# Kernel tuning notes

Hardware: AMD Instinct MI355X
Metric: run time of the kernel (lower is better)

Reference implementation:

```python
import jax, jax.numpy as jnp
import numpy as np

N_NODES = 100000
N_EDGES = 1600000
F = 64          # node_features (in == out for EvolveGCNO)
HID = 64        # hidden_size


def setup_inputs() -> dict:
    key = jax.random.key(0)
    ks = jax.random.split(key, 12)
    s = 1.0 / np.sqrt(F)
    inp = {
        "x": jax.random.normal(ks[0], (N_NODES, F), dtype=jnp.float32),
        "edge_index": jax.random.randint(ks[1], (2, N_EDGES), 0, N_NODES, dtype=jnp.int64),
        "edge_weight": jax.random.uniform(ks[2], (N_EDGES,), dtype=jnp.float32),
        # evolving GCN weight (initial_weight of EvolveGCNO)
        "W0": jax.random.uniform(ks[3], (F, F), jnp.float32, -s, s),
        # GRU (input_size=F, hidden_size=F): gates ordered r, z, n
        "gru_Wi": jax.random.uniform(ks[4], (3 * F, F), jnp.float32, -s, s),
        "gru_Wh": jax.random.uniform(ks[5], (3 * F, F), jnp.float32, -s, s),
        "gru_bi": jax.random.uniform(ks[6], (3 * F,), jnp.float32, -s, s),
        "gru_bh": jax.random.uniform(ks[7], (3 * F,), jnp.float32, -s, s),
        # projection F -> HID and head HID -> 1
        "proj_W": jax.random.uniform(ks[8], (HID, F), jnp.float32, -s, s),
        "proj_b": jax.random.uniform(ks[9], (HID,), jnp.float32, -s, s),
        "lin_W": jax.random.uniform(ks[10], (1, HID), jnp.float32, -1.0 / np.sqrt(HID), 1.0 / np.sqrt(HID)),
        "lin_b": jax.random.uniform(ks[11], (1,), jnp.float32, -1.0 / np.sqrt(HID), 1.0 / np.sqrt(HID)),
    }
    return inp


def reference(x, edge_index, edge_weight, W0, gru_Wi, gru_Wh, gru_bi, gru_bh,
              proj_W, proj_b, lin_W, lin_b):
    N = x.shape[0]
    # --- EvolveGCNO weight evolution: one GRU step, rows of W0 are both input and hidden ---
    gi = W0 @ gru_Wi.T + gru_bi  # [F, 3F]
    gh = W0 @ gru_Wh.T + gru_bh  # [F, 3F]
    i_r, i_z, i_n = jnp.split(gi, 3, axis=1)
    h_r, h_z, h_n = jnp.split(gh, 3, axis=1)
    r = jax.nn.sigmoid(i_r + h_r)
    z = jax.nn.sigmoid(i_z + h_z)
    n = jnp.tanh(i_n + r * h_n)
    W = (1.0 - z) * n + z * W0  # evolved GCN weight [F, F]

    # --- GCNConv with fixed evolved W: X' = D^-1/2 (A + I) D^-1/2 (X W) ---
    xw = x @ W  # [N, F]
    src, dst = edge_index[0], edge_index[1]
    loop = jnp.arange(N)
    src2 = jnp.concatenate([src, loop])
    dst2 = jnp.concatenate([dst, loop])
    w2 = jnp.concatenate([edge_weight, jnp.ones((N,), xw.dtype)])  # self-loop weight 1
    deg = jax.ops.segment_sum(w2, dst2, num_segments=N)
    dinv = jnp.where(deg > 0, jax.lax.rsqrt(deg), 0.0)
    norm = dinv[src2] * w2 * dinv[dst2]  # [E + N]
    h = jax.ops.segment_sum(xw[src2] * norm[:, None], dst2, num_segments=N)  # [N, F]

    # --- MLP head (dropout is identity in eval) ---
    h = jax.nn.relu(h @ proj_W.T + proj_b)
    return h @ lin_W.T + lin_b  # [N, 1]
```

## Files before the change

### kernel.cpp

```cpp
#include <hip/hip_runtime.h>
#include <stdint.h>

#define FDIM 64
#define BINSH 6
#define NBINS 1563
#define BCAP 1536
#define OVCAP 8192
#define PSTAGE 8192
#define PBLK 196
#define LSTRIDE 72

__device__ __forceinline__ float bf2f(unsigned int u) {
    union { float f; uint32_t i; } v; v.i = (u & 0xFFFFu) << 16; return v.f;
}
__device__ __forceinline__ unsigned short f2bf(float f) {
    union { float f; uint32_t i; } v; v.f = f;
    uint32_t u = v.i;
    u += 0x7FFFu + ((u >> 16) & 1u);
    return (unsigned short)(u >> 16);
}

__global__ __launch_bounds__(256) void k_sentinel(float* out, int N, float val) {
    int n = blockIdx.x * 256 + threadIdx.x;
    if (n < N) out[n] = (n == 0) ? val : 0.f;
}

__global__ __launch_bounds__(1024) void k_prep(
    const int* __restrict__ src, const int* __restrict__ dst,
    const float* __restrict__ ew, int* __restrict__ gcnt,
    int2* __restrict__ part, int* __restrict__ ovf_cnt,
    int* __restrict__ ovs, int* __restrict__ ovd, float* __restrict__ ovw, int E,
    const float* __restrict__ W0, const float* __restrict__ Wi,
    const float* __restrict__ Wh, const float* __restrict__ bi,
    const float* __restrict__ bh, const float* __restrict__ projW,
    float* __restrict__ M) {
    __shared__ char sm[12504];
    int t = threadIdx.x;
    if (blockIdx.x < PBLK) {
        int* hist = (int*)sm;
        int* lcur = hist + NBINS;
        for (int b = t; b < NBINS; b += 1024) hist[b] = 0;
        __syncthreads();
        int e0 = blockIdx.x * PSTAGE;
        int cnt = E - e0; if (cnt > PSTAGE) cnt = PSTAGE;
        for (int i = t; i < cnt; i += 1024) atomicAdd(&hist[dst[e0 + i] >> BINSH], 1);
        __syncthreads();
        for (int b = t; b < NBINS; b += 1024) {
            int h = hist[b];
            lcur[b] = h ? atomicAdd(&gcnt[b], h) : 0;
        }
        __syncthreads();
        for (int i = t; i < cnt; i += 1024) {
            int e = e0 + i;
            int d = dst[e];
            int b = d >> BINSH;
            int p = atomicAdd(&lcur[b], 1);
            if (p < BCAP) {
                part[(size_t)b * BCAP + p] = make_int2(src[e] | ((d & 63) << 20),
                                                       __float_as_int(ew[e]));
            } else {
                int op = atomicAdd(ovf_cnt, 1);
                if (op < OVCAP) {
                    ovs[op] = src[e];
                    ovd[op] = d;
                    ovw[op] = ew[e];
                }
            }
        }
    } else {
        int i = blockIdx.x - PBLK;
        float* w0s  = (float*)sm;
        float* wrow = w0s + 64;
        if (t < 64) w0s[t] = W0[i * 64 + t];
        __syncthreads();
        if (t < 64) {
            int j = t;
            float a0 = 0.f, a1 = 0.f, a2 = 0.f, b0 = 0.f, b1 = 0.f, b2 = 0.f;
#pragma unroll 8
            for (int k = 0; k < 64; k++) {
                float w0k = w0s[k];
                a0 += w0k * Wi[(j)       * 64 + k];
                a1 += w0k * Wi[(64 + j)  * 64 + k];
                a2 += w0k * Wi[(128 + j) * 64 + k];
                b0 += w0k * Wh[(j)       * 64 + k];
                b1 += w0k * Wh[(64 + j)  * 64 + k];
                b2 += w0k * Wh[(128 + j) * 64 + k];
            }
            float ir = a0 + bi[j],        hr = b0 + bh[j];
            float iz = a1 + bi[64 + j],   hz = b1 + bh[64 + j];
            float in_ = a2 + bi[128 + j], hn = b2 + bh[128 + j];
            float r = 1.f / (1.f + expf(-(ir + hr)));
            float z = 1.f / (1.f + expf(-(iz + hz)));
            float n = tanhf(in_ + r * hn);
            wrow[j] = (1.f - z) * n + z * w0s[j];
        }
        __syncthreads();
        if (t < 64) {
            float s = 0.f;
#pragma unroll 8
            for (int q = 0; q < 64; q++) s += wrow[q] * projW[t * 64 + q];
            M[i * 64 + t] = s;
        }
    }
}

__global__ __launch_bounds__(256) void k_xmdeg(
    const float* __restrict__ x, const float* __restrict__ M,
    unsigned short* __restrict__ xm, int N,
    const int* __restrict__ gcnt, const int2* __restrict__ part,
    const int* __restrict__ ovf_cnt, const int* __restrict__ ovd,
    const float* __restrict__ ovw, float* __restrict__ dinv,
    int* __restrict__ loffg) {
    __shared__ char sm[34816];
    int t = threadIdx.x;
    if (blockIdx.x < NBINS) {
        float* xs = (float*)sm;
        float* ms = xs + 64 * 68;
        int nb = blockIdx.x * 64;
#pragma unroll
        for (int i = 0; i < 4; i++) {
            int lin = i * 1024 + t * 4;
            int row = lin >> 6, col = lin & 63;
            int node = nb + row;
            float4 v = make_float4(0.f, 0.f, 0.f, 0.f);
            if (node < N) v = *(const float4*)(x + (size_t)node * 64 + col);
            *(float4*)&xs[row * 68 + col] = v;
            *(float4*)&ms[row * 68 + col] = *(const float4*)(M + lin);
        }
        __syncthreads();
        int tj = t & 15, tn = t >> 4;
        float acc[4][4] = {};
        for (int k = 0; k < 64; k += 4) {
            float4 xv[4], mv[4];
#pragma unroll
            for (int nn = 0; nn < 4; nn++) xv[nn] = *(const float4*)&xs[(tn * 4 + nn) * 68 + k];
#pragma unroll
            for (int kk = 0; kk < 4; kk++) mv[kk] = *(const float4*)&ms[(k + kk) * 68 + tj * 4];
#pragma unroll
            for (int nn = 0; nn < 4; nn++) {
                const float* xp = (const float*)&xv[nn];
#pragma unroll
                for (int kk = 0; kk < 4; kk++) {
                    float xk = xp[kk];
                    const float* mp = (const float*)&mv[kk];
                    acc[nn][0] += xk * mp[0];
                    acc[nn][1] += xk * mp[1];
                    acc[nn][2] += xk * mp[2];
                    acc[nn][3] += xk * mp[3];
                }
            }
        }
#pragma unroll
        for (int nn = 0; nn < 4; nn++) {
            int node = nb + tn * 4 + nn;
            if (node < N) {
                ushort4 o;
                o.x = f2bf(acc[nn][0]); o.y = f2bf(acc[nn][1]);
                o.z = f2bf(acc[nn][2]); o.w = f2bf(acc[nn][3]);
                *(ushort4*)&xm[(size_t)node * 64 + tj * 4] = o;
            }
        }
    } else {
        int b = blockIdx.x - NBINS;
        float* dl   = (float*)sm;
        int*   cntl = (int*)(dl + 64);
        int*   lofl = cntl + 64;
        if (t < 64) { dl[t] = 1.0f; cntl[t] = 0; }
        __syncthreads();
        int c = gcnt[b]; if (c > BCAP) c = BCAP;
        const int2* pe = part + (size_t)b * BCAP;
        for (int i = t; i < c; i += 256) {
            int2 e = pe[i];
            int nl = (e.x >> 20) & 63;
            atomicAdd(&dl[nl], __int_as_float(e.y));
            atomicAdd(&cntl[nl], 1);
        }
        int m = *ovf_cnt; if (m > OVCAP) m = OVCAP;
        for (int i = t; i < m; i += 256) {
            int d = ovd[i];
            if ((d >> BINSH) == b) atomicAdd(&dl[d & 63], ovw[i]);
        }
        __syncthreads();
        if (t == 0) {
            int o = 0;
#pragma unroll 16
            for (int k = 0; k < 64; k++) { lofl[k] = o; o += cntl[k]; }
            lofl[64] = o;
        }
        __syncthreads();
        if (t < 64) {
            int n = b * 64 + t;
            if (n < N) dinv[n] = rsqrtf(dl[t]);
        }
        if (t < 65) loffg[b * LSTRIDE + t] = lofl[t];
    }
}

__global__ __launch_bounds__(256) void k_gf(
    const unsigned short* __restrict__ xm, const float* __restrict__ dinv,
    const int* __restrict__ gcnt, const int2* __restrict__ part,
    const int* __restrict__ loffg,
    const float* __restrict__ projB, const float* __restrict__ linW,
    const float* __restrict__ linB, const int* __restrict__ ovf_cnt,
    const int* __restrict__ ovs, const int* __restrict__ ovd,
    const float* __restrict__ ovw, float* __restrict__ out, int N) {
    __shared__ int  loff[65];
    __shared__ int  lcur[64];
    __shared__ int2 ledge[BCAP];
    __shared__ float pbs[64], lws[64];
    int t = threadIdx.x, b = blockIdx.x;
    if (t < 65) loff[t] = loffg[b * LSTRIDE + t];
    if (t < 64) { pbs[t] = projB[t]; lws[t] = linW[t]; }
    __syncthreads();
    if (t < 64) lcur[t] = loff[t];
    __syncthreads();
    int c = gcnt[b]; if (c > BCAP) c = BCAP;
    const int2* pe = part + (size_t)b * BCAP;
    for (int i = t; i < c; i += 256) {
        int2 e = pe[i];
        int s = e.x & 0xFFFFF;
        float nw = dinv[s] * __int_as_float(e.y);
        int p = atomicAdd(&lcur[(e.x >> 20) & 63], 1);
        ledge[p] = make_int2(e.x, __float_as_int(nw));
    }
    __syncthreads();
    int m = *ovf_cnt; if (m > OVCAP) m = OVCAP;
    float lb = linB[0];
    int wv = t >> 6, lane = t & 63, eg = lane >> 4, fq = lane & 15, f = fq * 4;
    for (int nl = wv; nl < 64; nl += 4) {
        int n = b * 64 + nl;
        if (n >= N) continue;
        float dn = dinv[n];
        int beg = loff[nl], end = loff[nl + 1];
        float ax = 0.f, ay = 0.f, az = 0.f, aw = 0.f;
        float bx = 0.f, by = 0.f, bz = 0.f, bw = 0.f;
        int i = beg + eg;
        for (; i + 4 < end; i += 8) {
            int2 e0 = ledge[i];
            int2 e1 = ledge[i + 4];
            int s0 = e0.x & 0xFFFFF, s1 = e1.x & 0xFFFFF;
            uint2 u0 = *(const uint2*)&xm[(size_t)s0 * 64 + f];
            uint2 u1 = *(const uint2*)&xm[(size_t)s1 * 64 + f];
            float nm0 = __int_as_float(e0.y);
            float nm1 = __int_as_float(e1.y);
            ax += nm0 * bf2f(u0.x);       ay += nm0 * bf2f(u0.x >> 16);
            az += nm0 * bf2f(u0.y);       aw += nm0 * bf2f(u0.y >> 16);
            bx += nm1 * bf2f(u1.x);       by += nm1 * bf2f(u1.x >> 16);
            bz += nm1 * bf2f(u1.y);       bw += nm1 * bf2f(u1.y >> 16);
        }
        for (; i < end; i += 4) {
            int2 e = ledge[i];
            int s = e.x & 0xFFFFF;
            float nm = __int_as_float(e.y);
            uint2 u = *(const uint2*)&xm[(size_t)s * 64 + f];
            ax += nm * bf2f(u.x); ay += nm * bf2f(u.x >> 16);
            az += nm * bf2f(u.y); aw += nm * bf2f(u.y >> 16);
        }
        ax += bx; ay += by; az += bz; aw += bw;
        ax *= dn; ay *= dn; az *= dn; aw *= dn;
        ax += __shfl_xor(ax, 16); ay += __shfl_xor(ay, 16);
        az += __shfl_xor(az, 16); aw += __shfl_xor(aw, 16);
        ax += __shfl_xor(ax, 32); ay += __shfl_xor(ay, 32);
        az += __shfl_xor(az, 32); aw += __shfl_xor(aw, 32);
        if (eg == 0) {
            {
                uint2 u = *(const uint2*)&xm[(size_t)n * 64 + f];
                float sl = dn * dn;
                ax += sl * bf2f(u.x); ay += sl * bf2f(u.x >> 16);
                az += sl * bf2f(u.y); aw += sl * bf2f(u.y >> 16);
            }
            for (int q = 0; q < m; q++) {
                if (ovd[q] == n) {
                    int s = ovs[q];
                    float nm = dinv[s] * ovw[q] * dn;
                    uint2 u = *(const uint2*)&xm[(size_t)s * 64 + f];
                    ax += nm * bf2f(u.x); ay += nm * bf2f(u.x >> 16);
                    az += nm * bf2f(u.y); aw += nm * bf2f(u.y >> 16);
                }
            }
            float v0 = ax + pbs[f],     v1 = ay + pbs[f + 1];
            float v2 = az + pbs[f + 2], v3 = aw + pbs[f + 3];
            float s = (v0 > 0.f ? v0 : 0.f) * lws[f]
                    + (v1 > 0.f ? v1 : 0.f) * lws[f + 1]
                    + (v2 > 0.f ? v2 : 0.f) * lws[f + 2]
                    + (v3 > 0.f ? v3 : 0.f) * lws[f + 3];
            s += __shfl_xor(s, 1); s += __shfl_xor(s, 2);
            s += __shfl_xor(s, 4); s += __shfl_xor(s, 8);
            if (fq == 0) out[n] = s + lb;
        }
    }
}

extern "C" void kernel_launch(void* const* d_in, const int* in_sizes, int n_in,
                              void* d_out, int out_size, void* d_ws, size_t ws_size,
                              hipStream_t stream) {
    const float* x   = (const float*)d_in[0];
    const int*   ei  = (const int*)d_in[1];
    const float* ew  = (const float*)d_in[2];
    const float* W0  = (const float*)d_in[3];
    const float* gWi = (const float*)d_in[4];
    const float* gWh = (const float*)d_in[5];
    const float* gbi = (const float*)d_in[6];
    const float* gbh = (const float*)d_in[7];
    const float* pW  = (const float*)d_in[8];
    const float* pb  = (const float*)d_in[9];
    const float* lW  = (const float*)d_in[10];
    const float* lb  = (const float*)d_in[11];
    float* out = (float*)d_out;

    static const int EXPSZ[12] = {6400000, 3200000, 1600000, 4096, 12288, 12288,
                                  192, 192, 4096, 64, 64, 1};
    int mism = -1;
    for (int i = 0; i < 12 && i < n_in; i++)
        if (in_sizes[i] != EXPSZ[i]) { mism = i; break; }
    if (mism >= 0) {
        k_sentinel<<<(out_size + 255) / 256, 256, 0, stream>>>(out, out_size,
                                                               ldexpf(1.f, 30 + 3 * mism));
        return;
    }

    int N = in_sizes[0] / FDIM;
    int E = in_sizes[1] / 2;
    const int* src = ei;
    const int* dst = ei + E;

    char* wsb = (char*)d_ws;
    float* M       = (float*)(wsb);
    int*   gcnt    = (int*)  (wsb + (32u << 10));
    int*   ovf_cnt = (int*)  (wsb + (39u << 10));
    int*   ovs     = (int*)  (wsb + (44u << 10));
    int*   ovd     = (int*)  (wsb + (76u << 10));
    float* ovw     = (float*)(wsb + (108u << 10));
    float* dinv    = (float*)(wsb + (1u << 20));
    int*   loffg   = (int*)  (wsb + 1572864u);
    int2*  part    = (int2*) (wsb + (2u << 20));
    unsigned short* xm = (unsigned short*)(wsb + (22u << 20));

    hipMemsetAsync(gcnt, 0, (8u << 10), stream);

    k_prep<<<PBLK + 64, 1024, 0, stream>>>(src, dst, ew, gcnt, part,
                                           ovf_cnt, ovs, ovd, ovw, E,
                                           W0, gWi, gWh, gbi, gbh, pW, M);
    k_xmdeg<<<NBINS * 2, 256, 0, stream>>>(x, M, xm, N, gcnt, part,
                                           ovf_cnt, ovd, ovw, dinv, loffg);
    k_gf<<<NBINS, 256, 0, stream>>>(xm, dinv, gcnt, part, loffg, pb, lW, lb,
                                    ovf_cnt, ovs, ovd, ovw, out, N);
}
```

Before: 193.4 us.

## Stage edges in shared memory sorted by bin before coalesced partition writes

```diff
diff --git a/kernel.cpp b/kernel.cpp
--- a/kernel.cpp
+++ b/kernel.cpp
@@ -6,8 +6,8 @@
 #define NBINS 1563
 #define BCAP 1536
 #define OVCAP 8192
-#define PSTAGE 8192
-#define PBLK 196
+#define PSTAGE 4096
+#define PBLK 391
 #define LSTRIDE 72
 
 __device__ __forceinline__ float bf2f(unsigned int u) {
@@ -34,20 +34,50 @@
     const float* __restrict__ Wh, const float* __restrict__ bi,
     const float* __restrict__ bh, const float* __restrict__ projW,
     float* __restrict__ M) {
-    __shared__ char sm[12504];
+    __shared__ int  hist[NBINS];
+    __shared__ int  lcur[NBINS];
+    __shared__ int  wsum[16];
+    __shared__ int2 stage[PSTAGE];
+    __shared__ unsigned short sbin[PSTAGE];
     int t = threadIdx.x;
     if (blockIdx.x < PBLK) {
-        int* hist = (int*)sm;
-        int* lcur = hist + NBINS;
         for (int b = t; b < NBINS; b += 1024) hist[b] = 0;
         __syncthreads();
         int e0 = blockIdx.x * PSTAGE;
         int cnt = E - e0; if (cnt > PSTAGE) cnt = PSTAGE;
         for (int i = t; i < cnt; i += 1024) atomicAdd(&hist[dst[e0 + i] >> BINSH], 1);
         __syncthreads();
-        for (int b = t; b < NBINS; b += 1024) {
-            int h = hist[b];
-            lcur[b] = h ? atomicAdd(&gcnt[b], h) : 0;
+        int b0 = 2 * t, b1 = 2 * t + 1;
+        int h0 = (b0 < NBINS) ? hist[b0] : 0;
+        int h1 = (b1 < NBINS) ? hist[b1] : 0;
+        int s = h0 + h1;
+        int lane = t & 63, wid = t >> 6;
+        for (int off = 1; off < 64; off <<= 1) {
+            int v = __shfl_up(s, off);
+            if (lane >= off) s += v;
+        }
+        if (lane == 63) wsum[wid] = s;
+        __syncthreads();
+        if (t < 16) {
+            int v = wsum[t];
+            for (int off = 1; off < 16; off <<= 1) {
+                int u = __shfl_up(v, off);
+                if (t >= off) v += u;
+            }
+            wsum[t] = v;
+        }
+        __syncthreads();
+        int wbase = (wid == 0) ? 0 : wsum[wid - 1];
+        int excl = s + wbase - h0 - h1;
+        if (b0 < NBINS) {
+            int g0 = h0 ? atomicAdd(&gcnt[b0], h0) : 0;
+            lcur[b0] = excl;
+            hist[b0] = g0 - excl;
+        }
+        if (b1 < NBINS) {
+            int g1 = h1 ? atomicAdd(&gcnt[b1], h1) : 0;
+            lcur[b1] = excl + h0;
+            hist[b1] = g1 - (excl + h0);
         }
         __syncthreads();
         for (int i = t; i < cnt; i += 1024) {
@@ -55,21 +85,28 @@
             int d = dst[e];
             int b = d >> BINSH;
             int p = atomicAdd(&lcur[b], 1);
+            stage[p] = make_int2(src[e] | ((d & 63) << 20), __float_as_int(ew[e]));
+            sbin[p] = (unsigned short)b;
+        }
+        __syncthreads();
+        for (int i = t; i < cnt; i += 1024) {
+            int b = sbin[i];
+            int2 e = stage[i];
+            int p = i + hist[b];
             if (p < BCAP) {
-                part[(size_t)b * BCAP + p] = make_int2(src[e] | ((d & 63) << 20),
-                                                       __float_as_int(ew[e]));
+                part[(size_t)b * BCAP + p] = e;
             } else {
                 int op = atomicAdd(ovf_cnt, 1);
                 if (op < OVCAP) {
-                    ovs[op] = src[e];
-                    ovd[op] = d;
-                    ovw[op] = ew[e];
+                    ovs[op] = e.x & 0xFFFFF;
+                    ovd[op] = (b << BINSH) | ((e.x >> 20) & 63);
+                    ovw[op] = __int_as_float(e.y);
                 }
             }
         }
     } else {
         int i = blockIdx.x - PBLK;
-        float* w0s  = (float*)sm;
+        float* w0s  = (float*)hist;
         float* wrow = w0s + 64;
         if (t < 64) w0s[t] = W0[i * 64 + t];
         __syncthreads();
@@ -111,11 +148,9 @@
     const int* __restrict__ ovf_cnt, const int* __restrict__ ovd,
     const float* __restrict__ ovw, float* __restrict__ dinv,
     int* __restrict__ loffg) {
-    __shared__ char sm[34816];
+    __shared__ float xs[64 * 68];
     int t = threadIdx.x;
     if (blockIdx.x < NBINS) {
-        float* xs = (float*)sm;
-        float* ms = xs + 64 * 68;
         int nb = blockIdx.x * 64;
 #pragma unroll
         for (int i = 0; i < 4; i++) {
@@ -125,7 +160,6 @@
             float4 v = make_float4(0.f, 0.f, 0.f, 0.f);
             if (node < N) v = *(const float4*)(x + (size_t)node * 64 + col);
             *(float4*)&xs[row * 68 + col] = v;
-            *(float4*)&ms[row * 68 + col] = *(const float4*)(M + lin);
         }
         __syncthreads();
         int tj = t & 15, tn = t >> 4;
@@ -135,7 +169,7 @@
 #pragma unroll
             for (int nn = 0; nn < 4; nn++) xv[nn] = *(const float4*)&xs[(tn * 4 + nn) * 68 + k];
 #pragma unroll
-            for (int kk = 0; kk < 4; kk++) mv[kk] = *(const float4*)&ms[(k + kk) * 68 + tj * 4];
+            for (int kk = 0; kk < 4; kk++) mv[kk] = *(const float4*)(M + (k + kk) * 64 + tj * 4);
 #pragma unroll
             for (int nn = 0; nn < 4; nn++) {
                 const float* xp = (const float*)&xv[nn];
@@ -162,8 +196,8 @@
         }
     } else {
         int b = blockIdx.x - NBINS;
-        float* dl   = (float*)sm;
-        int*   cntl = (int*)(dl + 64);
+        float* dl   = xs;
+        int*   cntl = (int*)(xs + 64);
         int*   lofl = cntl + 64;
         if (t < 64) { dl[t] = 1.0f; cntl[t] = 0; }
         __syncthreads();
```

New measurement: 196.6 us. Within noise of the previous version (+1.6%).
